# Kernel optimization log

Measured on AMD Instinct MI355X. Metric: run time of the kernel, lower is better.

## Reference

```python
import jax, jax.numpy as jnp
import numpy as np

N, NA, LAYERS = 8, 4, 4
NTOT = N + NA
DIM = 2 ** NTOT
B = 1024

# Diagonal of the fixed CZ brick layer (CZ is diagonal, so one elementwise pass per layer).
# Qubit 0 is the most-significant bit of the state index (tensorcircuit convention).
def _cz_diag():
    idx = np.arange(DIM)
    bits = (idx[None, :] >> (NTOT - 1 - np.arange(NTOT)[:, None])) & 1  # [NTOT, DIM]
    par = np.zeros(DIM, dtype=np.int64)
    for i in range(NTOT // 2):
        par += bits[2 * i] * bits[2 * i + 1]
    for i in range((NTOT - 1) // 2):
        par += bits[2 * i + 1] * bits[2 * i + 2]
    return jnp.asarray(1.0 - 2.0 * (par % 2), dtype=jnp.complex64)

CZ_DIAG = _cz_diag()

def _apply_1q(state, U, q):
    # state: [B, DIM]; apply 2x2 unitary U on qubit q (batched over samples)
    l, r = 2 ** q, 2 ** (NTOT - q - 1)
    s = state.reshape(-1, l, 2, r)
    return jnp.einsum('ij,bljr->blir', U, s).reshape(-1, DIM)

def _back_circuit(state, params):
    # hardware-efficient ansatz: per layer RX,RY on every qubit, then CZ bricks
    for lay in range(LAYERS):
        off = 2 * NTOT * lay
        for q in range(NTOT):
            th = params[off + q] * 0.5
            c = jnp.cos(th).astype(jnp.complex64)
            ms = (-1j) * jnp.sin(th).astype(jnp.complex64)
            Rx = jnp.stack([jnp.stack([c, ms]), jnp.stack([ms, c])])
            state = _apply_1q(state, Rx, q)
            th = params[off + NTOT + q] * 0.5
            c, s = jnp.cos(th), jnp.sin(th)
            Ry = jnp.stack([jnp.stack([c, -s]), jnp.stack([s, c])]).astype(jnp.complex64)
            state = _apply_1q(state, Ry, q)
        state = state * CZ_DIAG
    return state

def setup_inputs() -> dict:
    key = jax.random.key(0)
    k1, k2, k3, k4 = jax.random.split(key, 4)
    return {
        'inputs_re': jax.random.normal(k1, (B, DIM), jnp.float32),
        'inputs_im': jax.random.normal(k2, (B, DIM), jnp.float32),
        'params': jax.random.normal(k3, (2 * NTOT * LAYERS,), jnp.float32),
        'u': jax.random.uniform(k4, (B,), jnp.float32),
    }

def reference(inputs_re, inputs_im, params, u):
    state = (inputs_re + 1j * inputs_im).astype(jnp.complex64)
    full = _back_circuit(state, params)                      # [B, 2^n_tot]
    s3 = full.reshape(B, 2 ** NA, 2 ** N)                    # [B, 2^na, 2^n]
    probs = jnp.sum(s3.real ** 2 + s3.imag ** 2, axis=2)     # ancilla outcome probs
    cdf = jnp.cumsum(probs, axis=1)
    thresh = u * cdf[:, -1]                                  # inverse-CDF multinomial
    m = jnp.argmax(cdf >= thresh[:, None], axis=1)           # [B] sampled outcome
    post = s3[jnp.arange(B), m]                              # [B, 2^n] collapsed state
    norm = jnp.sqrt(jnp.sum(post.real ** 2 + post.imag ** 2, axis=1, keepdims=True))
    post = post / norm
    return jnp.stack([post.real, post.imag], axis=-1)        # [B, 2^n, 2]
```

## Files before the change

kernel.cpp:

```cpp
#include <hip/hip_runtime.h>
#include <math.h>

#define NTOT   12
#define DIM    4096
#define LAYERS 4
#define NB     1024

typedef float v2f __attribute__((ext_vector_type(2)));

template<int G>
__device__ __forceinline__ void gate_pk(v2f (&x)[16], v2f P1, v2f P2) {
#pragma unroll
    for (int p = 0; p < 8; ++p) {
        const int j0 = ((p >> G) << (G + 1)) | (p & ((1 << G) - 1));
        const int j1 = j0 | (1 << G);
        const v2f x0 = x[j0], x1 = x[j1];
        v2f t, u;
        asm("v_pk_mul_f32 %0, %1, %2 op_sel:[1,1] op_sel_hi:[1,0] neg_hi:[1,0]"
            : "=v"(t) : "v"(P2), "v"(x1));
        asm("v_pk_fma_f32 %0, %1, %2, %0 op_sel:[1,0,0] op_sel_hi:[1,1,1] neg_lo:[1,0,0] neg_hi:[1,0,0]"
            : "+v"(t) : "v"(P1), "v"(x1));
        asm("v_pk_fma_f32 %0, %1, %2, %0 op_sel:[0,1,0] op_sel_hi:[0,0,1] neg_lo:[1,0,0]"
            : "+v"(t) : "v"(P2), "v"(x0));
        asm("v_pk_fma_f32 %0, %1, %2, %0 op_sel:[0,0,0] op_sel_hi:[0,1,1]"
            : "+v"(t) : "v"(P1), "v"(x0));
        asm("v_pk_mul_f32 %0, %1, %2 op_sel:[0,1] op_sel_hi:[0,0] neg_hi:[1,0]"
            : "=v"(u) : "v"(P2), "v"(x1));
        asm("v_pk_fma_f32 %0, %1, %2, %0 op_sel:[0,0,0] op_sel_hi:[0,1,1]"
            : "+v"(u) : "v"(P1), "v"(x1));
        asm("v_pk_fma_f32 %0, %1, %2, %0 op_sel:[1,1,0] op_sel_hi:[1,0,1] neg_hi:[1,0,0]"
            : "+v"(u) : "v"(P2), "v"(x0));
        asm("v_pk_fma_f32 %0, %1, %2, %0 op_sel:[1,0,0] op_sel_hi:[1,1,1]"
            : "+v"(u) : "v"(P1), "v"(x0));
        x[j0] = t; x[j1] = u;
    }
}

__global__ __launch_bounds__(256, 4) void qddpm_kernel(
    const float* __restrict__ in_re,
    const float* __restrict__ in_im,
    const float* __restrict__ params,
    const float* __restrict__ uu,
    float* __restrict__ out)
{
    __shared__ v2f    S[DIM];
    __shared__ float4 gco[48];
    __shared__ float  sprob[16];
    __shared__ int    ssel;
    __shared__ float  srnorm;

    const int b = blockIdx.x;
    const int t = threadIdx.x;

    {
        const float4* re4 = (const float4*)(in_re + (size_t)b * DIM);
        const float4* im4 = (const float4*)(in_im + (size_t)b * DIM);
#pragma unroll
        for (int k = 0; k < 4; ++k) {
            const int g  = k * 256 + t;
            const float4 vr = re4[g];
            const float4 vi = im4[g];
            const int i0 = g * 4;
            const int pb = i0 ^ ((i0 >> 4) & 15);
            S[pb ^ 0] = (v2f){vr.x, vi.x};
            S[pb ^ 1] = (v2f){vr.y, vi.y};
            S[pb ^ 2] = (v2f){vr.z, vi.z};
            S[pb ^ 3] = (v2f){vr.w, vi.w};
        }
        if (t < 48) {
            const int lay = t / 12, q = t - lay * 12;
            float c1, s1, c2, s2;
            sincosf(params[lay * 24 + q] * 0.5f, &s1, &c1);
            sincosf(params[lay * 24 + 12 + q] * 0.5f, &s2, &c2);
            gco[t] = make_float4(c1 * c2, c1 * s2, s1 * s2, s1 * c2);
        }
    }
    __syncthreads();

    const int baseA = t ^ ((t >> 4) & 15);
    const int hiB = t >> 4, loB = t & 15;
    const int baseC = t * 16, mC = t & 15;

    int smask = 0;
#pragma unroll
    for (int j = 0; j < 16; ++j) {
        const int i = t * 16 + j;
        smask |= (__popc(i & (i >> 1) & 0x7FF) & 1) << j;
    }

    v2f x[16];
    v2f acc2 = (v2f){0.0f, 0.0f};

#pragma unroll 1
    for (int lay = 0; lay < LAYERS; ++lay) {
        const int gb = lay * 12;

#pragma unroll
        for (int j = 0; j < 16; ++j) x[j] = S[j * 256 + baseA];
        { float4 c;
          c = gco[gb + 3]; gate_pk<0>(x, (v2f){c.x,c.y}, (v2f){c.z,c.w});
          c = gco[gb + 2]; gate_pk<1>(x, (v2f){c.x,c.y}, (v2f){c.z,c.w});
          c = gco[gb + 1]; gate_pk<2>(x, (v2f){c.x,c.y}, (v2f){c.z,c.w});
          c = gco[gb + 0]; gate_pk<3>(x, (v2f){c.x,c.y}, (v2f){c.z,c.w}); }
#pragma unroll
        for (int j = 0; j < 16; ++j) S[j * 256 + baseA] = x[j];
        __syncthreads();

#pragma unroll
        for (int j = 0; j < 16; ++j) x[j] = S[hiB * 256 + j * 16 + (loB ^ j)];
        { float4 c;
          c = gco[gb + 7]; gate_pk<0>(x, (v2f){c.x,c.y}, (v2f){c.z,c.w});
          c = gco[gb + 6]; gate_pk<1>(x, (v2f){c.x,c.y}, (v2f){c.z,c.w});
          c = gco[gb + 5]; gate_pk<2>(x, (v2f){c.x,c.y}, (v2f){c.z,c.w});
          c = gco[gb + 4]; gate_pk<3>(x, (v2f){c.x,c.y}, (v2f){c.z,c.w}); }
#pragma unroll
        for (int j = 0; j < 16; ++j) S[hiB * 256 + j * 16 + (loB ^ j)] = x[j];
        __syncthreads();

#pragma unroll
        for (int j = 0; j < 16; ++j) x[j] = S[baseC + (j ^ mC)];
        { float4 c;
          c = gco[gb + 11]; gate_pk<0>(x, (v2f){c.x,c.y}, (v2f){c.z,c.w});
          c = gco[gb + 10]; gate_pk<1>(x, (v2f){c.x,c.y}, (v2f){c.z,c.w});
          c = gco[gb +  9]; gate_pk<2>(x, (v2f){c.x,c.y}, (v2f){c.z,c.w});
          c = gco[gb +  8]; gate_pk<3>(x, (v2f){c.x,c.y}, (v2f){c.z,c.w}); }
#pragma unroll
        for (int j = 0; j < 16; ++j) {
            if (smask & (1 << j)) x[j] = -x[j];
        }
        if (lay == LAYERS - 1) {
#pragma unroll
            for (int j = 0; j < 16; ++j) acc2 += x[j] * x[j];
        }
#pragma unroll
        for (int j = 0; j < 16; ++j) S[baseC + (j ^ mC)] = x[j];
        __syncthreads();
    }

    float partial = acc2.x + acc2.y;
#pragma unroll
    for (int o = 8; o > 0; o >>= 1)
        partial += __shfl_down(partial, o, 16);
    if ((t & 15) == 0) sprob[t >> 4] = partial;
    __syncthreads();

    if (t == 0) {
        float cdf[16];
        float a = 0.0f;
#pragma unroll
        for (int i = 0; i < 16; ++i) { a += sprob[i]; cdf[i] = a; }
        const float thresh = uu[b] * a;
        int m = 0;
        for (int i = 0; i < 16; ++i) { if (cdf[i] >= thresh) { m = i; break; } }
        ssel = m;
        srnorm = 1.0f / sqrtf(sprob[m]);
    }
    __syncthreads();

    {
        const int m = ssel;
        const float rn = srnorm;
        const v2f a = S[m * 256 + baseA];
        ((float2*)out)[(size_t)b * 256 + t] = make_float2(a.x * rn, a.y * rn);
    }
}

extern "C" void kernel_launch(void* const* d_in, const int* in_sizes, int n_in,
                              void* d_out, int out_size, void* d_ws, size_t ws_size,
                              hipStream_t stream) {
    const float* in_re  = (const float*)d_in[0];
    const float* in_im  = (const float*)d_in[1];
    const float* params = (const float*)d_in[2];
    const float* u      = (const float*)d_in[3];
    float* out = (float*)d_out;
    qddpm_kernel<<<NB, 256, 0, stream>>>(in_re, in_im, params, u, out);
}
```

Measured before the change: 111.6 us.

## Replace XOR-swizzled shared layout with padded layout and vectorized accesses

Shared memory changes from an XOR swizzle to a padded layout (two extra elements per 16, 288 per 256-row), so the third-stage loads and stores and the initial fill can use 128-bit float4 accesses. It also replaces the sign-flip branch with bit XORs, folds the probability reduction into the last layer's barrier, and has every thread compute the sampling redundantly, which removes two block barriers. The cost is about 4.5KB more LDS per block, which could lower occupancy, plus possible bank conflicts with the new strides.

Measured after the change: 110.8 us. No clear change (-0.7%).

```diff
diff --git a/kernel.cpp b/kernel.cpp
--- a/kernel.cpp
+++ b/kernel.cpp
@@ -5,6 +5,7 @@
 #define DIM    4096
 #define LAYERS 4
 #define NB     1024
+#define SPAD   4608
 
 typedef float v2f __attribute__((ext_vector_type(2)));
 
@@ -43,14 +44,13 @@
     const float* __restrict__ uu,
     float* __restrict__ out)
 {
-    __shared__ v2f    S[DIM];
+    __shared__ v2f    S[SPAD];
     __shared__ float4 gco[48];
     __shared__ float  sprob[16];
-    __shared__ int    ssel;
-    __shared__ float  srnorm;
 
     const int b = blockIdx.x;
     const int t = threadIdx.x;
+    const float uval = uu[b];
 
     {
         const float4* re4 = (const float4*)(in_re + (size_t)b * DIM);
@@ -60,12 +60,10 @@
             const int g  = k * 256 + t;
             const float4 vr = re4[g];
             const float4 vi = im4[g];
-            const int i0 = g * 4;
-            const int pb = i0 ^ ((i0 >> 4) & 15);
-            S[pb ^ 0] = (v2f){vr.x, vi.x};
-            S[pb ^ 1] = (v2f){vr.y, vi.y};
-            S[pb ^ 2] = (v2f){vr.z, vi.z};
-            S[pb ^ 3] = (v2f){vr.w, vi.w};
+            const int pb = g * 4 + (g >> 2) * 2;
+            float4* dst = (float4*)(S + pb);
+            dst[0] = make_float4(vr.x, vi.x, vr.y, vi.y);
+            dst[1] = make_float4(vr.z, vi.z, vr.w, vi.w);
         }
         if (t < 48) {
             const int lay = t / 12, q = t - lay * 12;
@@ -75,50 +73,64 @@
             gco[t] = make_float4(c1 * c2, c1 * s2, s1 * s2, s1 * c2);
         }
     }
-    __syncthreads();
 
-    const int baseA = t ^ ((t >> 4) & 15);
-    const int hiB = t >> 4, loB = t & 15;
-    const int baseC = t * 16, mC = t & 15;
+    const int baseA = t + 2 * (t >> 4);
+    const int baseB = (t >> 4) * 288 + (t & 15);
+    const int baseC = t * 18;
 
-    int smask = 0;
+    int sw[16];
 #pragma unroll
     for (int j = 0; j < 16; ++j) {
         const int i = t * 16 + j;
-        smask |= (__popc(i & (i >> 1) & 0x7FF) & 1) << j;
+        sw[j] = (__popc(i & (i >> 1) & 0x7FF) & 1) << 31;
     }
 
     v2f x[16];
     v2f acc2 = (v2f){0.0f, 0.0f};
+
+    __syncthreads();
 
 #pragma unroll 1
     for (int lay = 0; lay < LAYERS; ++lay) {
         const int gb = lay * 12;
 
 #pragma unroll
-        for (int j = 0; j < 16; ++j) x[j] = S[j * 256 + baseA];
+        for (int j = 0; j < 16; ++j) x[j] = S[baseA + 288 * j];
         { float4 c;
           c = gco[gb + 3]; gate_pk<0>(x, (v2f){c.x,c.y}, (v2f){c.z,c.w});
           c = gco[gb + 2]; gate_pk<1>(x, (v2f){c.x,c.y}, (v2f){c.z,c.w});
           c = gco[gb + 1]; gate_pk<2>(x, (v2f){c.x,c.y}, (v2f){c.z,c.w});
           c = gco[gb + 0]; gate_pk<3>(x, (v2f){c.x,c.y}, (v2f){c.z,c.w}); }
 #pragma unroll
-        for (int j = 0; j < 16; ++j) S[j * 256 + baseA] = x[j];
+        for (int j = 0; j < 16; ++j) S[baseA + 288 * j] = x[j];
         __syncthreads();
 
 #pragma unroll
-        for (int j = 0; j < 16; ++j) x[j] = S[hiB * 256 + j * 16 + (loB ^ j)];
+        for (int j = 0; j < 16; ++j) x[j] = S[baseB + 18 * j];
         { float4 c;
           c = gco[gb + 7]; gate_pk<0>(x, (v2f){c.x,c.y}, (v2f){c.z,c.w});
           c = gco[gb + 6]; gate_pk<1>(x, (v2f){c.x,c.y}, (v2f){c.z,c.w});
           c = gco[gb + 5]; gate_pk<2>(x, (v2f){c.x,c.y}, (v2f){c.z,c.w});
           c = gco[gb + 4]; gate_pk<3>(x, (v2f){c.x,c.y}, (v2f){c.z,c.w}); }
 #pragma unroll
-        for (int j = 0; j < 16; ++j) S[hiB * 256 + j * 16 + (loB ^ j)] = x[j];
+        for (int j = 0; j < 16; ++j) S[baseB + 18 * j] = x[j];
         __syncthreads();
 
+        {
+            const float4* src = (const float4*)(S + baseC);
 #pragma unroll
-        for (int j = 0; j < 16; ++j) x[j] = S[baseC + (j ^ mC)];
+            for (int q = 0; q < 4; ++q) {
+                const float4 v = src[q];
+                x[2 * q]     = (v2f){v.x, v.y};
+                x[2 * q + 1] = (v2f){v.z, v.w};
+            }
+#pragma unroll
+            for (int q = 4; q < 8; ++q) {
+                const float4 v = src[q];
+                x[2 * q]     = (v2f){v.x, v.y};
+                x[2 * q + 1] = (v2f){v.z, v.w};
+            }
+        }
         { float4 c;
           c = gco[gb + 11]; gate_pk<0>(x, (v2f){c.x,c.y}, (v2f){c.z,c.w});
           c = gco[gb + 10]; gate_pk<1>(x, (v2f){c.x,c.y}, (v2f){c.z,c.w});
@@ -126,42 +138,41 @@
           c = gco[gb +  8]; gate_pk<3>(x, (v2f){c.x,c.y}, (v2f){c.z,c.w}); }
 #pragma unroll
         for (int j = 0; j < 16; ++j) {
-            if (smask & (1 << j)) x[j] = -x[j];
+            x[j].x = __uint_as_float(__float_as_uint(x[j].x) ^ sw[j]);
+            x[j].y = __uint_as_float(__float_as_uint(x[j].y) ^ sw[j]);
         }
         if (lay == LAYERS - 1) {
 #pragma unroll
             for (int j = 0; j < 16; ++j) acc2 += x[j] * x[j];
         }
+        {
+            float4* dst = (float4*)(S + baseC);
 #pragma unroll
-        for (int j = 0; j < 16; ++j) S[baseC + (j ^ mC)] = x[j];
+            for (int q = 0; q < 8; ++q)
+                dst[q] = make_float4(x[2 * q].x, x[2 * q].y, x[2 * q + 1].x, x[2 * q + 1].y);
+        }
+        if (lay == LAYERS - 1) {
+            float partial = acc2.x + acc2.y;
+#pragma unroll
+            for (int o = 8; o > 0; o >>= 1)
+                partial += __shfl_down(partial, o, 16);
+            if ((t & 15) == 0) sprob[t >> 4] = partial;
+        }
         __syncthreads();
     }
 
-    float partial = acc2.x + acc2.y;
-#pragma unroll
-    for (int o = 8; o > 0; o >>= 1)
-        partial += __shfl_down(partial, o, 16);
-    if ((t & 15) == 0) sprob[t >> 4] = partial;
-    __syncthreads();
-
-    if (t == 0) {
-        float cdf[16];
+    float cdf[16];
+    {
         float a = 0.0f;
 #pragma unroll
         for (int i = 0; i < 16; ++i) { a += sprob[i]; cdf[i] = a; }
-        const float thresh = uu[b] * a;
+        const float thresh = uval * a;
         int m = 0;
-        for (int i = 0; i < 16; ++i) { if (cdf[i] >= thresh) { m = i; break; } }
-        ssel = m;
-        srnorm = 1.0f / sqrtf(sprob[m]);
-    }
-    __syncthreads();
-
-    {
-        const int m = ssel;
-        const float rn = srnorm;
-        const v2f a = S[m * 256 + baseA];
-        ((float2*)out)[(size_t)b * 256 + t] = make_float2(a.x * rn, a.y * rn);
+#pragma unroll
+        for (int i = 15; i >= 0; --i) { if (cdf[i] >= thresh) m = i; }
+        const float rn = 1.0f / sqrtf(sprob[m]);
+        const v2f amp = S[baseA + 288 * m];
+        ((float2*)out)[(size_t)b * 256 + t] = make_float2(amp.x * rn, amp.y * rn);
     }
 }
 
```
